# Kernel tuning notes

Hardware: AMD Instinct MI355X
Metric: run time of the kernel (lower is better)

The kernel has to match this reference:

```python
import jax, jax.numpy as jnp
import numpy as np

P_DROP = 0.2
N_NODES = 100000
N_EDGES = 1600000
IN_DIM, HID_DIM, OUT_DIM = 128, 128, 64


def sage_conv(x, src, dst, Wl, Wr, b, n_nodes):
    # PyG SAGEConv (aggr='mean', root_weight=True):
    #   out_i = W_l @ mean_{j in N(i)} x_j + W_r @ x_i + b
    msgs = jnp.take(x, src, axis=0)                                   # [E, d]
    agg = jax.ops.segment_sum(msgs, dst, num_segments=n_nodes)        # [N, d]
    cnt = jax.ops.segment_sum(jnp.ones((src.shape[0],), x.dtype), dst,
                              num_segments=n_nodes)                   # [N]
    agg = agg / jnp.maximum(cnt, 1.0)[:, None]                        # mean, 0 for isolated nodes
    return agg @ Wl + x @ Wr + b


def setup_inputs() -> dict:
    key = jax.random.key(0)
    ks = jax.random.split(key, 8)
    x = jax.random.normal(ks[0], (N_NODES, IN_DIM), dtype=jnp.float32)
    edge_index = jax.random.randint(ks[1], (2, N_EDGES), 0, N_NODES, dtype=jnp.int32)
    drop_u = jax.random.uniform(ks[2], (N_NODES, HID_DIM), dtype=jnp.float32)
    s1 = 1.0 / np.sqrt(IN_DIM)
    s2 = 1.0 / np.sqrt(HID_DIM)
    W1l = jax.random.normal(ks[3], (IN_DIM, HID_DIM), dtype=jnp.float32) * s1
    W1r = jax.random.normal(ks[4], (IN_DIM, HID_DIM), dtype=jnp.float32) * s1
    b1 = jnp.zeros((HID_DIM,), dtype=jnp.float32)
    W2l = jax.random.normal(ks[5], (HID_DIM, OUT_DIM), dtype=jnp.float32) * s2
    W2r = jax.random.normal(ks[6], (HID_DIM, OUT_DIM), dtype=jnp.float32) * s2
    b2 = jnp.zeros((OUT_DIM,), dtype=jnp.float32)
    return {"x": x, "edge_index": edge_index, "drop_u": drop_u,
            "W1l": W1l, "W1r": W1r, "b1": b1,
            "W2l": W2l, "W2r": W2r, "b2": b2}


def reference(x, edge_index, drop_u, W1l, W1r, b1, W2l, W2r, b2):
    n = x.shape[0]
    src, dst = edge_index[0], edge_index[1]
    h = jax.nn.elu(sage_conv(x, src, dst, W1l, W1r, b1, n))
    keep = (drop_u >= P_DROP).astype(h.dtype) / (1.0 - P_DROP)  # inverted dropout, p=0.2
    h = h * keep
    h = jax.nn.elu(sage_conv(h, src, dst, W2l, W2r, b2, n))
    return h
```

## Files before the change

kernel.cpp:

```cpp
#include <hip/hip_runtime.h>
#include <cstdint>
#include <cstddef>

#define TPB 256
#define BCAP 2560
#define NBKMAX 800
#define EPB 8192

typedef short bf16x8 __attribute__((ext_vector_type(8)));
typedef float f32x4 __attribute__((ext_vector_type(4)));

__device__ __forceinline__ unsigned short f2bf(float f) {
  unsigned int u = __float_as_uint(f);
  unsigned int r = (u + 0x7fffu + ((u >> 16) & 1u)) >> 16;
  return (unsigned short)r;
}
__device__ __forceinline__ float bf2f(unsigned short h) {
  return __uint_as_float(((unsigned int)h) << 16);
}

__device__ __forceinline__ void gload16(const void* g, void* l) {
  __builtin_amdgcn_global_load_lds(
      (const __attribute__((address_space(1))) unsigned int*)g,
      (__attribute__((address_space(3))) unsigned int*)l, 16, 0, 0);
}

template <int N>
__device__ __forceinline__ void waitvm() {
  asm volatile("s_waitcnt vmcnt(%0)" ::"n"(N) : "memory");
}


__global__ __launch_bounds__(256) void multisplit_scatter(
    const int* __restrict__ src, const int* __restrict__ dst,
    unsigned int* __restrict__ be, int* __restrict__ bcnt, int e, int nbk) {
  __shared__ int hist[NBKMAX];
  __shared__ int curs[NBKMAX];
  int tx = threadIdx.x;
  int e0 = blockIdx.x * EPB;
  int e1 = min(e, e0 + EPB);

  for (int b = tx; b < nbk; b += TPB) hist[b] = 0;
  __syncthreads();
  for (int i = e0 + tx; i < e1; i += TPB) atomicAdd(&hist[dst[i] >> 7], 1);
  __syncthreads();
  int rot = (blockIdx.x * 131) % nbk;
  for (int s = tx; s < nbk; s += TPB) {
    int b = s + rot;
    if (b >= nbk) b -= nbk;
    int h = hist[b];
    curs[b] = (h > 0) ? atomicAdd(&bcnt[b], h) : 0;
  }
  __syncthreads();
  for (int i = e0 + tx; i < e1; i += TPB) {
    int d = dst[i];
    int b = d >> 7;
    int p = atomicAdd(&curs[b], 1);
    if (p < BCAP)
      be[(size_t)b * BCAP + p] = ((unsigned int)(d & 127) << 17) | (unsigned int)src[i];
  }
}

__global__ void bucket_scan(const int* __restrict__ bcnt, int* __restrict__ bbase, int nbk) {
  __shared__ int s[TPB];
  __shared__ int carry;
  int tx = threadIdx.x;
  if (tx == 0) carry = 0;
  __syncthreads();
  for (int base = 0; base < nbk; base += TPB) {
    int i = base + tx;
    int v = (i < nbk) ? bcnt[i] : 0;
    s[tx] = v;
    __syncthreads();
    for (int d = 1; d < TPB; d <<= 1) {
      int t = (tx >= d) ? s[tx - d] : 0;
      __syncthreads();
      s[tx] += t;
      __syncthreads();
    }
    int c = carry;
    if (i < nbk) bbase[i] = c + s[tx] - v;
    __syncthreads();
    if (tx == TPB - 1) carry = c + s[tx];
    __syncthreads();
  }
}

__global__ __launch_bounds__(256) void per_bucket_build(
    const unsigned int* __restrict__ be, const int* __restrict__ bcnt,
    const int* __restrict__ bbase, int* __restrict__ off, int* __restrict__ col,
    int n, int e) {
  int b = blockIdx.x, tx = threadIdx.x;
  int cnt = bcnt[b];
  if (cnt > BCAP) cnt = BCAP;
  int base = bbase[b];
  int node0 = b << 7;
  __shared__ int scnt[128];
  __shared__ int sscan[128];
  if (tx < 128) scnt[tx] = 0;
  __syncthreads();
  const unsigned int* eb = be + (size_t)b * BCAP;
  for (int i = tx; i < cnt; i += 256) atomicAdd(&scnt[eb[i] >> 17], 1);
  __syncthreads();
  if (tx < 128) sscan[tx] = scnt[tx];
  __syncthreads();
  for (int d = 1; d < 128; d <<= 1) {
    int t = 0;
    if (tx < 128 && tx >= d) t = sscan[tx - d];
    __syncthreads();
    if (tx < 128) sscan[tx] += t;
    __syncthreads();
  }
  if (tx < 128) {
    int excl = sscan[tx] - scnt[tx];
    if (node0 + tx < n) off[node0 + tx] = base + excl;
    scnt[tx] = excl;
  }
  if (b == 0 && tx == 0) off[n] = e;
  __syncthreads();
  for (int i = tx; i < cnt; i += 256) {
    unsigned int u = eb[i];
    int p = atomicAdd(&scnt[u >> 17], 1);
    col[base + p] = (int)(u & 0x1ffff);
  }
}


__global__ void f32_to_bf16_v4(const float* __restrict__ in, unsigned short* __restrict__ out,
                               int n4) {
  int i = blockIdx.x * TPB + threadIdx.x;
  if (i >= n4) return;
  float4 v = ((const float4*)in)[i];
  ushort4 o;
  o.x = f2bf(v.x); o.y = f2bf(v.y); o.z = f2bf(v.z); o.w = f2bf(v.w);
  ((ushort4*)out)[i] = o;
}

__global__ void make_dropmask(const float* __restrict__ u, unsigned char* __restrict__ m,
                              int n4) {
  int i = blockIdx.x * TPB + threadIdx.x;
  if (i >= n4) return;
  float4 v = ((const float4*)u)[i];
  uchar4 o;
  o.x = (v.x >= 0.2f) ? 1 : 0;
  o.y = (v.y >= 0.2f) ? 1 : 0;
  o.z = (v.z >= 0.2f) ? 1 : 0;
  o.w = (v.w >= 0.2f) ? 1 : 0;
  ((uchar4*)m)[i] = o;
}

template <int NF>
__global__ void build_wt(const float* __restrict__ Wl, const float* __restrict__ Wr,
                         unsigned short* __restrict__ Wt) {
  int idx = blockIdx.x * TPB + threadIdx.x;
  if (idx >= NF * 256) return;
  int nn = idx >> 8;
  int k = idx & 255;
  float v = (k < 128) ? Wl[k * NF + nn] : Wr[(k - 128) * NF + nn];
  Wt[idx] = f2bf(v);
}


__global__ void aggregate_bf(const unsigned short* __restrict__ X,
                             const int* __restrict__ off, const int* __restrict__ col,
                             unsigned short* __restrict__ out, int n) {
  int wv = (blockIdx.x * TPB + threadIdx.x) >> 6;
  int lane = threadIdx.x & 63;
  int li = lane & 15;
  int node = wv * 4 + (lane >> 4);
  bool alive = node < n;
  int s0 = 0, s1 = 0;
  if (alive) {
    s0 = off[node];
    s1 = off[node + 1];
  }
  int cnt = s1 - s0;

  float a0 = 0.f, a1 = 0.f, a2 = 0.f, a3 = 0.f,
        a4 = 0.f, a5 = 0.f, a6 = 0.f, a7 = 0.f;

  for (int base = 0; base < cnt; base += 16) {
    int idx = s0 + base + li;
    int ci = col[min(idx, s1 - 1)];
    int lim = cnt - base;
#pragma unroll
    for (int j = 0; j < 16; ++j) {
      int c = __shfl(ci, j, 16);
      const uint4* p = (const uint4*)(X + (size_t)c * 128 + li * 8);
      uint4 v = *p;
      float s = (j < lim) ? 1.f : 0.f;
      a0 = fmaf(s, __uint_as_float(v.x << 16), a0);
      a1 = fmaf(s, __uint_as_float(v.x & 0xffff0000u), a1);
      a2 = fmaf(s, __uint_as_float(v.y << 16), a2);
      a3 = fmaf(s, __uint_as_float(v.y & 0xffff0000u), a3);
      a4 = fmaf(s, __uint_as_float(v.z << 16), a4);
      a5 = fmaf(s, __uint_as_float(v.z & 0xffff0000u), a5);
      a6 = fmaf(s, __uint_as_float(v.w << 16), a6);
      a7 = fmaf(s, __uint_as_float(v.w & 0xffff0000u), a7);
    }
  }

  if (alive) {
    float inv = (cnt > 0) ? 1.0f / (float)cnt : 0.f;
    uint4 o;
    o.x = ((unsigned int)f2bf(a1 * inv) << 16) | f2bf(a0 * inv);
    o.y = ((unsigned int)f2bf(a3 * inv) << 16) | f2bf(a2 * inv);
    o.z = ((unsigned int)f2bf(a5 * inv) << 16) | f2bf(a4 * inv);
    o.w = ((unsigned int)f2bf(a7 * inv) << 16) | f2bf(a6 * inv);
    *(uint4*)(out + (size_t)node * 128 + li * 8) = o;
  }
}


template <int NFTOT, bool DROP, bool OUT32>
__global__ __launch_bounds__(256) void gemm_mfma(
    const unsigned short* __restrict__ A1, const unsigned short* __restrict__ A2,
    const unsigned short* __restrict__ Wt, const float* __restrict__ bias,
    const unsigned char* __restrict__ dmask, unsigned short* __restrict__ outb,
    float* __restrict__ outf, int n) {
  constexpr int IPC = 6;
  __shared__ __align__(16) unsigned short sA[2][128 * 64];
  __shared__ __align__(16) unsigned short sB[2][64 * 64];

  int tid = threadIdx.x;
  int row0 = blockIdx.x * 128;
  int ncol0 = blockIdx.y * 64;
  int lane = tid & 63;
  int wid = tid >> 6;
  int wm = wid >> 1, wn = wid & 1;
  int lq = lane & 15, q = lane >> 4;

  int sr = tid >> 3, sc8 = tid & 7;
  int cg = sc8 ^ (sr & 7);

  int arow[4];
#pragma unroll
  for (int t = 0; t < 4; ++t) arow[t] = min(row0 + sr + t * 32, n - 1);

  f32x4 acc[4][2];
#pragma unroll
  for (int i = 0; i < 4; ++i)
#pragma unroll
    for (int j = 0; j < 2; ++j) acc[i][j] = (f32x4)(0.f);

  auto issue = [&](int c, int b) {
    const unsigned short* Asrc = (c < 2) ? A1 : A2;
    int koff = (c & 1) * 64;
#pragma unroll
    for (int t = 0; t < 4; ++t) {
      gload16(Asrc + (size_t)arow[t] * 128 + koff + cg * 8,
              (char*)sA[b] + t * 4096 + wid * 1024);
    }
#pragma unroll
    for (int t = 0; t < 2; ++t) {
      gload16(Wt + (size_t)(ncol0 + sr + t * 32) * 256 + c * 64 + cg * 8,
              (char*)sB[b] + t * 4096 + wid * 1024);
    }
  };

  issue(0, 0);
  issue(1, 1);

#pragma unroll
  for (int c = 0; c < 4; ++c) {
    if (c < 3) waitvm<IPC>(); else waitvm<0>();
    __builtin_amdgcn_s_barrier();
    __builtin_amdgcn_sched_barrier(0);

    const int buf = c & 1;
#pragma unroll
    for (int ks = 0; ks < 2; ++ks) {
      bf16x8 a[4], b[2];
#pragma unroll
      for (int i = 0; i < 4; ++i) {
        int rr = wm * 64 + i * 16 + lq;
        a[i] = *(const bf16x8*)(&sA[buf][rr * 64 + (((ks * 4 + q) ^ (rr & 7)) * 8)]);
      }
#pragma unroll
      for (int j = 0; j < 2; ++j) {
        int rb = wn * 32 + j * 16 + lq;
        b[j] = *(const bf16x8*)(&sB[buf][rb * 64 + (((ks * 4 + q) ^ (rb & 7)) * 8)]);
      }
#pragma unroll
      for (int i = 0; i < 4; ++i)
#pragma unroll
        for (int j = 0; j < 2; ++j)
          acc[i][j] = __builtin_amdgcn_mfma_f32_16x16x32_bf16(a[i], b[j], acc[i][j], 0, 0, 0);
    }

    if (c < 2) {
      asm volatile("s_waitcnt lgkmcnt(0)" ::: "memory");
      __builtin_amdgcn_sched_barrier(0);
      __builtin_amdgcn_s_barrier();
      issue(c + 2, buf);
    }
  }

#pragma unroll
  for (int j = 0; j < 2; ++j) {
    int gcol = ncol0 + wn * 32 + j * 16 + lq;
    float bv = bias[gcol];
#pragma unroll
    for (int i = 0; i < 4; ++i) {
      int rbase = row0 + wm * 64 + i * 16 + q * 4;
#pragma unroll
      for (int r = 0; r < 4; ++r) {
        int row = rbase + r;
        if (row >= n) continue;
        float v = acc[i][j][r] + bv;
        v = (v > 0.f) ? v : expm1f(v);
        if (DROP) {
          unsigned char k = dmask[(size_t)row * 128 + gcol];
          v = k ? v * 1.25f : 0.f;
        }
        if (OUT32) outf[(size_t)row * NFTOT + gcol] = v;
        else outb[(size_t)row * NFTOT + gcol] = f2bf(v);
      }
    }
  }
}


extern "C" void kernel_launch(void* const* d_in, const int* in_sizes, int n_in,
                              void* d_out, int out_size, void* d_ws, size_t ws_size,
                              hipStream_t stream) {
  const float* x = (const float*)d_in[0];
  const int* ei = (const int*)d_in[1];
  const float* dropu = (const float*)d_in[2];
  const float* W1l = (const float*)d_in[3];
  const float* W1r = (const float*)d_in[4];
  const float* b1 = (const float*)d_in[5];
  const float* W2l = (const float*)d_in[6];
  const float* W2r = (const float*)d_in[7];
  const float* b2 = (const float*)d_in[8];

  int n = in_sizes[0] / 128;
  int e = in_sizes[1] / 2;
  const int* src = ei;
  const int* dst = ei + e;
  float* out = (float*)d_out;

  char* w = (char*)d_ws;
  auto alloc = [&](size_t bytes) -> char* {
    char* p = w;
    w += (bytes + 255) & ~(size_t)255;
    return p;
  };
  int nbk = (n + 127) / 128;
  int* off = (int*)alloc((size_t)(n + 1) * sizeof(int));
  int* col = (int*)alloc((size_t)e * sizeof(int));
  int* bcnt = (int*)alloc((size_t)nbk * sizeof(int));
  int* bbase = (int*)alloc((size_t)nbk * sizeof(int));
  unsigned short* xb = (unsigned short*)alloc((size_t)n * 128 * 2);
  unsigned short* hb = (unsigned short*)alloc((size_t)n * 128 * 2);
  unsigned short* aggb = (unsigned short*)alloc((size_t)n * 128 * 2);
  unsigned char* dmask = (unsigned char*)alloc((size_t)n * 128);
  unsigned short* Wt1 = (unsigned short*)alloc(128 * 256 * 2);
  unsigned short* Wt2 = (unsigned short*)alloc(64 * 256 * 2);
  unsigned int* be = (unsigned int*)aggb;

  hipMemsetAsync(bcnt, 0, (size_t)nbk * sizeof(int), stream);

  int gMS = (e + EPB - 1) / EPB;
  multisplit_scatter<<<gMS, TPB, 0, stream>>>(src, dst, be, bcnt, e, nbk);
  bucket_scan<<<1, TPB, 0, stream>>>(bcnt, bbase, nbk);
  per_bucket_build<<<nbk, TPB, 0, stream>>>(be, bcnt, bbase, off, col, n, e);

  int n4 = n * 128 / 4;
  f32_to_bf16_v4<<<(n4 + TPB - 1) / TPB, TPB, 0, stream>>>(x, xb, n4);
  make_dropmask<<<(n4 + TPB - 1) / TPB, TPB, 0, stream>>>(dropu, dmask, n4);
  build_wt<128><<<(128 * 256 + TPB - 1) / TPB, TPB, 0, stream>>>(W1l, W1r, Wt1);
  build_wt<64><<<(64 * 256 + TPB - 1) / TPB, TPB, 0, stream>>>(W2l, W2r, Wt2);

  int gAgg = ((n + 3) / 4 * 64 + TPB - 1) / TPB;
  int gR = (n + 127) / 128;

  aggregate_bf<<<gAgg, TPB, 0, stream>>>(xb, off, col, aggb, n);
  gemm_mfma<128, true, false><<<dim3(gR, 2), TPB, 0, stream>>>(aggb, xb, Wt1, b1, dmask, hb, nullptr, n);

  aggregate_bf<<<gAgg, TPB, 0, stream>>>(hb, off, col, aggb, n);
  gemm_mfma<64, false, true><<<dim3(gR, 1), TPB, 0, stream>>>(aggb, hb, Wt2, b2, nullptr, nullptr, out, n);
}
```

Measured before the change: 444.8 us.

## Reorder layer-2 as project-then-aggregate and process two nodes per lane group

Layer 2 now multiplies h by both W2l and W2r first, producing a 64-wide bf16 projection P and an fp32 root term Q, then mean-aggregates the narrower P over neighbours and fuses bias, root add and ELU into the aggregation. This halves the bytes gathered per edge in the second aggregation, since the gather drops from 128 to 64 features per row. The layer-1 aggregation also handles two nodes per 16-lane group to raise memory-level parallelism. The cost is an extra fp32 Q buffer round trip, higher register pressure, and bf16 rounding of P before the sum, which slightly changes numerics.

```diff
diff --git a/kernel.cpp b/kernel.cpp
--- a/kernel.cpp
+++ b/kernel.cpp
@@ -160,6 +160,16 @@
   Wt[idx] = f2bf(v);
 }
 
+__global__ void build_wt2p(const float* __restrict__ W2l, const float* __restrict__ W2r,
+                           unsigned short* __restrict__ Wt) {
+  int idx = blockIdx.x * TPB + threadIdx.x;
+  if (idx >= 128 * 128) return;
+  int nn = idx >> 7;
+  int k = idx & 127;
+  float v = (nn < 64) ? W2l[k * 64 + nn] : W2r[k * 64 + (nn - 64)];
+  Wt[idx] = f2bf(v);
+}
+
 
 __global__ void aggregate_bf(const unsigned short* __restrict__ X,
                              const int* __restrict__ off, const int* __restrict__ col,
@@ -167,27 +177,95 @@
   int wv = (blockIdx.x * TPB + threadIdx.x) >> 6;
   int lane = threadIdx.x & 63;
   int li = lane & 15;
-  int node = wv * 4 + (lane >> 4);
+  int g = lane >> 4;
+  int nA = wv * 8 + g;
+  int nB = wv * 8 + 4 + g;
+  bool alA = nA < n, alB = nB < n;
+  int s0A = 0, s1A = 0, s0B = 0, s1B = 0;
+  if (alA) { s0A = off[nA]; s1A = off[nA + 1]; }
+  if (alB) { s0B = off[nB]; s1B = off[nB + 1]; }
+  int cntA = s1A - s0A, cntB = s1B - s0B;
+  int cmax = max(cntA, cntB);
+
+  float aA0 = 0.f, aA1 = 0.f, aA2 = 0.f, aA3 = 0.f,
+        aA4 = 0.f, aA5 = 0.f, aA6 = 0.f, aA7 = 0.f;
+  float aB0 = 0.f, aB1 = 0.f, aB2 = 0.f, aB3 = 0.f,
+        aB4 = 0.f, aB5 = 0.f, aB6 = 0.f, aB7 = 0.f;
+
+  for (int base = 0; base < cmax; base += 16) {
+    int ciA = col[max(0, min(s0A + base + li, s1A - 1))];
+    int ciB = col[max(0, min(s0B + base + li, s1B - 1))];
+    int limA = cntA - base, limB = cntB - base;
+#pragma unroll
+    for (int j = 0; j < 16; ++j) {
+      int cA = __shfl(ciA, j, 16);
+      int cB = __shfl(ciB, j, 16);
+      uint4 vA = *(const uint4*)(X + (size_t)cA * 128 + li * 8);
+      uint4 vB = *(const uint4*)(X + (size_t)cB * 128 + li * 8);
+      float sA = (j < limA) ? 1.f : 0.f;
+      float sB = (j < limB) ? 1.f : 0.f;
+      aA0 = fmaf(sA, __uint_as_float(vA.x << 16), aA0);
+      aA1 = fmaf(sA, __uint_as_float(vA.x & 0xffff0000u), aA1);
+      aA2 = fmaf(sA, __uint_as_float(vA.y << 16), aA2);
+      aA3 = fmaf(sA, __uint_as_float(vA.y & 0xffff0000u), aA3);
+      aA4 = fmaf(sA, __uint_as_float(vA.z << 16), aA4);
+      aA5 = fmaf(sA, __uint_as_float(vA.z & 0xffff0000u), aA5);
+      aA6 = fmaf(sA, __uint_as_float(vA.w << 16), aA6);
+      aA7 = fmaf(sA, __uint_as_float(vA.w & 0xffff0000u), aA7);
+      aB0 = fmaf(sB, __uint_as_float(vB.x << 16), aB0);
+      aB1 = fmaf(sB, __uint_as_float(vB.x & 0xffff0000u), aB1);
+      aB2 = fmaf(sB, __uint_as_float(vB.y << 16), aB2);
+      aB3 = fmaf(sB, __uint_as_float(vB.y & 0xffff0000u), aB3);
+      aB4 = fmaf(sB, __uint_as_float(vB.z << 16), aB4);
+      aB5 = fmaf(sB, __uint_as_float(vB.z & 0xffff0000u), aB5);
+      aB6 = fmaf(sB, __uint_as_float(vB.w << 16), aB6);
+      aB7 = fmaf(sB, __uint_as_float(vB.w & 0xffff0000u), aB7);
+    }
+  }
+
+  if (alA) {
+    float inv = (cntA > 0) ? 1.0f / (float)cntA : 0.f;
+    uint4 o;
+    o.x = ((unsigned int)f2bf(aA1 * inv) << 16) | f2bf(aA0 * inv);
+    o.y = ((unsigned int)f2bf(aA3 * inv) << 16) | f2bf(aA2 * inv);
+    o.z = ((unsigned int)f2bf(aA5 * inv) << 16) | f2bf(aA4 * inv);
+    o.w = ((unsigned int)f2bf(aA7 * inv) << 16) | f2bf(aA6 * inv);
+    *(uint4*)(out + (size_t)nA * 128 + li * 8) = o;
+  }
+  if (alB) {
+    float inv = (cntB > 0) ? 1.0f / (float)cntB : 0.f;
+    uint4 o;
+    o.x = ((unsigned int)f2bf(aB1 * inv) << 16) | f2bf(aB0 * inv);
+    o.y = ((unsigned int)f2bf(aB3 * inv) << 16) | f2bf(aB2 * inv);
+    o.z = ((unsigned int)f2bf(aB5 * inv) << 16) | f2bf(aB4 * inv);
+    o.w = ((unsigned int)f2bf(aB7 * inv) << 16) | f2bf(aB6 * inv);
+    *(uint4*)(out + (size_t)nB * 128 + li * 8) = o;
+  }
+}
+
+
+__global__ void aggregate_add(const unsigned short* __restrict__ P,
+                              const int* __restrict__ off, const int* __restrict__ col,
+                              const float* __restrict__ Q, float* __restrict__ out, int n) {
+  int wv = (blockIdx.x * TPB + threadIdx.x) >> 6;
+  int lane = threadIdx.x & 63;
+  int li = lane & 7;
+  int node = wv * 8 + (lane >> 3);
   bool alive = node < n;
   int s0 = 0, s1 = 0;
-  if (alive) {
-    s0 = off[node];
-    s1 = off[node + 1];
-  }
+  if (alive) { s0 = off[node]; s1 = off[node + 1]; }
   int cnt = s1 - s0;
 
   float a0 = 0.f, a1 = 0.f, a2 = 0.f, a3 = 0.f,
         a4 = 0.f, a5 = 0.f, a6 = 0.f, a7 = 0.f;
 
-  for (int base = 0; base < cnt; base += 16) {
-    int idx = s0 + base + li;
-    int ci = col[min(idx, s1 - 1)];
+  for (int base = 0; base < cnt; base += 8) {
+    int ci = col[max(0, min(s0 + base + li, s1 - 1))];
     int lim = cnt - base;
 #pragma unroll
-    for (int j = 0; j < 16; ++j) {
-      int c = __shfl(ci, j, 16);
-      const uint4* p = (const uint4*)(X + (size_t)c * 128 + li * 8);
-      uint4 v = *p;
+    for (int j = 0; j < 8; ++j) {
+      int c = __shfl(ci, j, 8);
+      uint4 v = *(const uint4*)(P + (size_t)c * 64 + li * 8);
       float s = (j < lim) ? 1.f : 0.f;
       a0 = fmaf(s, __uint_as_float(v.x << 16), a0);
       a1 = fmaf(s, __uint_as_float(v.x & 0xffff0000u), a1);
@@ -202,23 +280,35 @@
 
   if (alive) {
     float inv = (cnt > 0) ? 1.0f / (float)cnt : 0.f;
-    uint4 o;
-    o.x = ((unsigned int)f2bf(a1 * inv) << 16) | f2bf(a0 * inv);
-    o.y = ((unsigned int)f2bf(a3 * inv) << 16) | f2bf(a2 * inv);
-    o.z = ((unsigned int)f2bf(a5 * inv) << 16) | f2bf(a4 * inv);
-    o.w = ((unsigned int)f2bf(a7 * inv) << 16) | f2bf(a6 * inv);
-    *(uint4*)(out + (size_t)node * 128 + li * 8) = o;
-  }
-}
-
-
-template <int NFTOT, bool DROP, bool OUT32>
+    const float4* qp = (const float4*)(Q + (size_t)node * 64 + li * 8);
+    float4 q0 = qp[0], q1 = qp[1];
+    float4 o0, o1;
+    o0.x = a0 * inv + q0.x; o0.y = a1 * inv + q0.y;
+    o0.z = a2 * inv + q0.z; o0.w = a3 * inv + q0.w;
+    o1.x = a4 * inv + q1.x; o1.y = a5 * inv + q1.y;
+    o1.z = a6 * inv + q1.z; o1.w = a7 * inv + q1.w;
+    o0.x = (o0.x > 0.f) ? o0.x : expm1f(o0.x);
+    o0.y = (o0.y > 0.f) ? o0.y : expm1f(o0.y);
+    o0.z = (o0.z > 0.f) ? o0.z : expm1f(o0.z);
+    o0.w = (o0.w > 0.f) ? o0.w : expm1f(o0.w);
+    o1.x = (o1.x > 0.f) ? o1.x : expm1f(o1.x);
+    o1.y = (o1.y > 0.f) ? o1.y : expm1f(o1.y);
+    o1.z = (o1.z > 0.f) ? o1.z : expm1f(o1.z);
+    o1.w = (o1.w > 0.f) ? o1.w : expm1f(o1.w);
+    float4* op = (float4*)(out + (size_t)node * 64 + li * 8);
+    op[0] = o0; op[1] = o1;
+  }
+}
+
+
+template <int NCH, int MODE>
 __global__ __launch_bounds__(256) void gemm_mfma(
     const unsigned short* __restrict__ A1, const unsigned short* __restrict__ A2,
     const unsigned short* __restrict__ Wt, const float* __restrict__ bias,
     const unsigned char* __restrict__ dmask, unsigned short* __restrict__ outb,
     float* __restrict__ outf, int n) {
   constexpr int IPC = 6;
+  constexpr int KTOT = NCH * 64;
   __shared__ __align__(16) unsigned short sA[2][128 * 64];
   __shared__ __align__(16) unsigned short sB[2][64 * 64];
 
@@ -253,7 +343,7 @@
     }
 #pragma unroll
     for (int t = 0; t < 2; ++t) {
-      gload16(Wt + (size_t)(ncol0 + sr + t * 32) * 256 + c * 64 + cg * 8,
+      gload16(Wt + (size_t)(ncol0 + sr + t * 32) * KTOT + c * 64 + cg * 8,
               (char*)sB[b] + t * 4096 + wid * 1024);
     }
   };
@@ -262,8 +352,8 @@
   issue(1, 1);
 
 #pragma unroll
-  for (int c = 0; c < 4; ++c) {
-    if (c < 3) waitvm<IPC>(); else waitvm<0>();
+  for (int c = 0; c < NCH; ++c) {
+    if (c < NCH - 1) waitvm<IPC>(); else waitvm<0>();
     __builtin_amdgcn_s_barrier();
     __builtin_amdgcn_sched_barrier(0);
 
@@ -288,7 +378,7 @@
           acc[i][j] = __builtin_amdgcn_mfma_f32_16x16x32_bf16(a[i], b[j], acc[i][j], 0, 0, 0);
     }
 
-    if (c < 2) {
+    if (c < NCH - 2) {
       asm volatile("s_waitcnt lgkmcnt(0)" ::: "memory");
       __builtin_amdgcn_sched_barrier(0);
       __builtin_amdgcn_s_barrier();
@@ -299,7 +389,9 @@
 #pragma unroll
   for (int j = 0; j < 2; ++j) {
     int gcol = ncol0 + wn * 32 + j * 16 + lq;
-    float bv = bias[gcol];
+    float bv;
+    if (MODE == 0) bv = bias[gcol];
+    else bv = (gcol >= 64) ? bias[gcol - 64] : 0.f;
 #pragma unroll
     for (int i = 0; i < 4; ++i) {
       int rbase = row0 + wm * 64 + i * 16 + q * 4;
@@ -308,13 +400,15 @@
         int row = rbase + r;
         if (row >= n) continue;
         float v = acc[i][j][r] + bv;
-        v = (v > 0.f) ? v : expm1f(v);
-        if (DROP) {
+        if (MODE == 0) {
+          v = (v > 0.f) ? v : expm1f(v);
           unsigned char k = dmask[(size_t)row * 128 + gcol];
           v = k ? v * 1.25f : 0.f;
+          outb[(size_t)row * 128 + gcol] = f2bf(v);
+        } else {
+          if (gcol < 64) outb[(size_t)row * 64 + gcol] = f2bf(v);
+          else outf[(size_t)row * 64 + (gcol - 64)] = v;
         }
-        if (OUT32) outf[(size_t)row * NFTOT + gcol] = v;
-        else outb[(size_t)row * NFTOT + gcol] = f2bf(v);
       }
     }
   }
@@ -356,8 +450,10 @@
   unsigned short* aggb = (unsigned short*)alloc((size_t)n * 128 * 2);
   unsigned char* dmask = (unsigned char*)alloc((size_t)n * 128);
   unsigned short* Wt1 = (unsigned short*)alloc(128 * 256 * 2);
-  unsigned short* Wt2 = (unsigned short*)alloc(64 * 256 * 2);
+  unsigned short* Wt2 = (unsigned short*)alloc(128 * 128 * 2);
   unsigned int* be = (unsigned int*)aggb;
+  unsigned short* pb = xb;
+  float* qf = (float*)aggb;
 
   hipMemsetAsync(bcnt, 0, (size_t)nbk * sizeof(int), stream);
 
@@ -370,14 +466,14 @@
   f32_to_bf16_v4<<<(n4 + TPB - 1) / TPB, TPB, 0, stream>>>(x, xb, n4);
   make_dropmask<<<(n4 + TPB - 1) / TPB, TPB, 0, stream>>>(dropu, dmask, n4);
   build_wt<128><<<(128 * 256 + TPB - 1) / TPB, TPB, 0, stream>>>(W1l, W1r, Wt1);
-  build_wt<64><<<(64 * 256 + TPB - 1) / TPB, TPB, 0, stream>>>(W2l, W2r, Wt2);
-
-  int gAgg = ((n + 3) / 4 * 64 + TPB - 1) / TPB;
+  build_wt2p<<<(128 * 128 + TPB - 1) / TPB, TPB, 0, stream>>>(W2l, W2r, Wt2);
+
+  int gAgg = (n + 31) / 32;
   int gR = (n + 127) / 128;
 
   aggregate_bf<<<gAgg, TPB, 0, stream>>>(xb, off, col, aggb, n);
-  gemm_mfma<128, true, false><<<dim3(gR, 2), TPB, 0, stream>>>(aggb, xb, Wt1, b1, dmask, hb, nullptr, n);
-
-  aggregate_bf<<<gAgg, TPB, 0, stream>>>(hb, off, col, aggb, n);
-  gemm_mfma<64, false, true><<<dim3(gR, 1), TPB, 0, stream>>>(aggb, hb, Wt2, b2, nullptr, nullptr, out, n);
-}
+  gemm_mfma<4, 0><<<dim3(gR, 2), TPB, 0, stream>>>(aggb, xb, Wt1, b1, dmask, hb, nullptr, n);
+
+  gemm_mfma<2, 1><<<dim3(gR, 2), TPB, 0, stream>>>(hb, nullptr, Wt2, b2, nullptr, pb, qf, n);
+  aggregate_add<<<gAgg, TPB, 0, stream>>>(pb, off, col, qf, out, n);
+}
```

New measurement: 478.8 us. 7.6% more time.
